# Kernel tuning notes

Measured on AMD Instinct MI355X. Metric: run time of the kernel, lower is better.

The kernel has to match this reference:

```python
import jax, jax.numpy as jnp
import numpy as np

# Nemotron-H Mamba2 mixer decoder layer (prefill path, zero initial states,
# full context lengths). Dims per init_kwargs.
B, S, H = 1, 256, 4096
NH, P, G, N, K = 128, 64, 8, 128, 4   # num_heads, head_dim, n_groups, ssm_state_size, conv_kernel
D_INNER = NH * P                      # 8192
D_STATE = G * N                       # 1024
CONV_DIM = D_INNER + 2 * D_STATE      # 10240
IN_OUT = D_INNER + CONV_DIM + NH      # 18560
EPS = 1e-6


def setup_inputs() -> dict:
    key = jax.random.key(0)
    ks = jax.random.split(key, 8)
    sc = 0.02
    return {
        "hidden_states": jax.random.normal(ks[0], (B, S, H), jnp.float32),
        "conv_state": jnp.zeros((B, CONV_DIM, K - 1), jnp.float32),
        "ssm_state": jnp.zeros((B, NH, P, N), jnp.float32),
        "norm_weight": jnp.ones((H,), jnp.float32),
        "w_in": jax.random.normal(ks[1], (IN_OUT, H), jnp.float32) * sc,
        "conv_w": jax.random.normal(ks[2], (CONV_DIM, K), jnp.float32) * 0.2,
        "conv_b": jnp.zeros((CONV_DIM,), jnp.float32),
        "A_log": jax.random.uniform(ks[3], (NH,), jnp.float32, 0.0, 1.0),
        "D_param": jax.random.normal(ks[4], (NH,), jnp.float32) * 0.1,
        "dt_bias": jax.random.normal(ks[5], (NH,), jnp.float32) * 0.1,
        "ssm_norm_weight": jnp.ones((D_INNER,), jnp.float32),
        "w_out": jax.random.normal(ks[6], (H, D_INNER), jnp.float32) * sc,
    }


def _rmsnorm(x, w, eps=EPS):
    var = jnp.mean(x * x, axis=-1, keepdims=True)
    return x * jax.lax.rsqrt(var + eps) * w


def reference(hidden_states, conv_state, ssm_state, norm_weight, w_in, conv_w,
              conv_b, A_log, D_param, dt_bias, ssm_norm_weight, w_out):
    resid = hidden_states
    h = _rmsnorm(hidden_states, norm_weight)           # pre-mixer RMSNorm
    proj = jnp.einsum('bsh,oh->bso', h, w_in)          # in_proj [B,S,18560]
    gate = proj[..., :D_INNER]
    xconv = proj[..., D_INNER:D_INNER + CONV_DIM]
    dt = proj[..., D_INNER + CONV_DIM:]                # [B,S,NH]

    # depthwise causal conv1d, initial left context = conv_state
    xc = jnp.swapaxes(xconv, 1, 2)                     # [B,CONV_DIM,S]
    xpad = jnp.concatenate([conv_state, xc], axis=-1)  # [B,CONV_DIM,S+K-1]
    conv_state_out = xpad[:, :, -(K - 1):]
    y = conv_b[None, :, None]
    for j in range(K):                                 # K=4 taps, unrolled
        y = y + conv_w[:, j][None, :, None] * xpad[:, :, j:j + S]
    y = jax.nn.silu(jnp.swapaxes(y, 1, 2))             # [B,S,CONV_DIM]

    xs = y[..., :D_INNER].reshape(B, S, NH, P)
    Bs = y[..., D_INNER:D_INNER + D_STATE].reshape(B, S, G, N)
    Cs = y[..., D_INNER + D_STATE:].reshape(B, S, G, N)

    A = -jnp.exp(A_log)                                # [NH]
    dtp = jax.nn.softplus(dt + dt_bias)                # [B,S,NH]
    rep = NH // G
    Bh = jnp.repeat(Bs, rep, axis=2)                   # [B,S,NH,N]
    Ch = jnp.repeat(Cs, rep, axis=2)

    def step(state, inp):
        x_t, b_t, c_t, dt_t = inp                      # [B,NH,P],[B,NH,N],[B,NH,N],[B,NH]
        dA = jnp.exp(dt_t * A)                         # [B,NH]
        state = state * dA[..., None, None] + (dt_t[..., None] * x_t)[..., None] * b_t[:, :, None, :]
        y_t = jnp.einsum('bhpn,bhn->bhp', state, c_t)
        return state, y_t

    inps = (jnp.swapaxes(xs, 0, 1), jnp.swapaxes(Bh, 0, 1),
            jnp.swapaxes(Ch, 0, 1), jnp.swapaxes(dtp, 0, 1))
    ssm_state_out, ys = jax.lax.scan(step, ssm_state, inps)
    ys = jnp.swapaxes(ys, 0, 1) + D_param[None, None, :, None] * xs
    ssm_out = ys.reshape(B, S, D_INNER)

    # gated grouped RMSNorm (group_size = D_INNER // G = 1024)
    gated = ssm_out * jax.nn.silu(gate)
    gsize = D_INNER // G
    gg = gated.reshape(B, S, D_INNER // gsize, gsize)
    var = jnp.mean(gg * gg, axis=-1, keepdims=True)
    normed = (gg * jax.lax.rsqrt(var + EPS)).reshape(B, S, D_INNER) * ssm_norm_weight

    out = jnp.einsum('bsd,hd->bsh', normed, w_out)     # out_proj
    return resid + out, conv_state_out, ssm_state_out
```

## Files before the change

### kernel.cpp

```cpp
#include <hip/hip_runtime.h>
#include <hip/hip_bf16.h>

#define Sq 256
#define Hd 4096
#define NH 128
#define Pd 64
#define Gg 8
#define Nn 128
#define D_INNER 8192
#define D_STATE 1024
#define CONV_DIM 10240
#define IN_OUT 18560
#define DT_COL0 18432
#define EPSI 1e-6f

typedef _Float16 f16x8 __attribute__((ext_vector_type(8)));
typedef _Float16 f16x2 __attribute__((ext_vector_type(2)));
typedef float f32x4 __attribute__((ext_vector_type(4)));

__device__ inline ushort f2h(float f) {
  _Float16 h = (_Float16)f;
  return __builtin_bit_cast(ushort, h);
}
__device__ inline float h2f(ushort u) {
  return (float)__builtin_bit_cast(_Float16, u);
}
__device__ inline ushort f2h_lo(float f, ushort hi) {
  float hf = (float)__builtin_bit_cast(_Float16, hi);
  _Float16 l = (_Float16)(f - hf);
  return __builtin_bit_cast(ushort, l);
}
__device__ inline f16x2 pkrtz(float a, float b) {
  return __builtin_bit_cast(f16x2, __builtin_amdgcn_cvt_pkrtz(a, b));
}

__global__ __launch_bounds__(256) void rmsnorm_k(const float* __restrict__ x,
                                                 const float* __restrict__ w,
                                                 ushort* __restrict__ h_hi,
                                                 ushort* __restrict__ h_lo) {
  int s = blockIdx.x, t = threadIdx.x;
  const float4* row = reinterpret_cast<const float4*>(x + (size_t)s * Hd);
  const float4* wv  = reinterpret_cast<const float4*>(w);
  float4 v[4];
  float ss = 0.f;
#pragma unroll
  for (int i = 0; i < 4; i++) {
    v[i] = row[t + i * 256];
    ss += v[i].x * v[i].x + v[i].y * v[i].y + v[i].z * v[i].z + v[i].w * v[i].w;
  }
#pragma unroll
  for (int off = 32; off > 0; off >>= 1) ss += __shfl_xor(ss, off);
  __shared__ float red[4];
  if ((t & 63) == 0) red[t >> 6] = ss;
  __syncthreads();
  ss = red[0] + red[1] + red[2] + red[3];
  float scale = rsqrtf(ss * (1.f / (float)Hd) + EPSI);
  ushort4* hh = reinterpret_cast<ushort4*>(h_hi + (size_t)s * Hd);
  ushort4* hl = reinterpret_cast<ushort4*>(h_lo + (size_t)s * Hd);
#pragma unroll
  for (int i = 0; i < 4; i++) {
    float4 wi = wv[t + i * 256];
    float f0 = v[i].x * scale * wi.x, f1 = v[i].y * scale * wi.y;
    float f2 = v[i].z * scale * wi.z, f3 = v[i].w * scale * wi.w;
    ushort4 oh, ol;
    oh.x = f2h(f0); ol.x = f2h_lo(f0, oh.x);
    oh.y = f2h(f1); ol.y = f2h_lo(f1, oh.y);
    oh.z = f2h(f2); ol.z = f2h_lo(f2, oh.z);
    oh.w = f2h(f3); ol.w = f2h_lo(f3, oh.w);
    hh[t + i * 256] = oh;
    hl[t + i * 256] = ol;
  }
}

__global__ __launch_bounds__(512) void gemm_8p(const ushort* __restrict__ A,
                                               const float* __restrict__ B,
                                               float* __restrict__ C0,
                                               ushort* __restrict__ Cp,
                                               int ldc, int K, int kLen) {
  __shared__ __align__(16) ushort As[2][256 * 64];
  __shared__ __align__(16) ushort Bs[2][64 * 64];
  int t = threadIdx.x;
  int wave = t >> 6, lane = t & 63;
  int wr = wave >> 1, wc = wave & 1;
  int frow = lane & 15, gq = lane >> 4;
  int bcol = blockIdx.x * 64;
  int z = blockIdx.z;
  int kStart = z * kLen;

  int agl = (lane & 7) ^ (lane >> 3);
  const ushort* ApG = A + (size_t)(wave * 8 + (lane >> 3)) * K + kStart + agl * 8;

  int brow = t >> 3, bgp = t & 7;
  int bgl = bgp ^ (brow & 7);
  const float* BpG = B + (size_t)(bcol + brow) * K + kStart + bgl * 8;
  int bDst = brow * 128 + bgp * 16;

  f32x4 acc[4][2] = {};
  float4 rb[2];
  const int NT = kLen / 64;

#define SB() __builtin_amdgcn_sched_barrier(0)
#define ISSUE_RB(kk) { rb[0] = *(const float4*)(BpG + (kk)); \
                       rb[1] = *(const float4*)(BpG + (kk) + 4); }
#define DMA_A4(buf, kk) { _Pragma("unroll") for (int p = 0; p < 4; ++p) \
    __builtin_amdgcn_global_load_lds( \
        (const __attribute__((address_space(1))) void*)(ApG + (size_t)p * 64 * K + (kk)), \
        (__attribute__((address_space(3))) void*)((char*)&As[0][0] + (buf) * 32768 + p * 8192 + wave * 1024), \
        16, 0, 0); }
#define WRITE_RB(buf) { union { f16x2 h2[4]; uint4 q; } u; \
    u.h2[0] = pkrtz(rb[0].x, rb[0].y); u.h2[1] = pkrtz(rb[0].z, rb[0].w); \
    u.h2[2] = pkrtz(rb[1].x, rb[1].y); u.h2[3] = pkrtz(rb[1].z, rb[1].w); \
    *(uint4*)((char*)&Bs[0][0] + (buf) * 8192 + bDst) = u.q; }
#define PHASE(cur, kh) { \
    f16x8 afp[4], bfp[2]; \
    _Pragma("unroll") for (int m = 0; m < 4; ++m) { \
      int row = wr * 64 + m * 16 + frow; \
      afp[m] = *(const f16x8*)((const char*)&As[0][0] + (cur) * 32768 + row * 128 + \
                               (((((kh) << 2) | gq) ^ (row & 7)) << 4)); } \
    _Pragma("unroll") for (int n = 0; n < 2; ++n) { \
      int row = wc * 32 + n * 16 + frow; \
      bfp[n] = *(const f16x8*)((const char*)&Bs[0][0] + (cur) * 8192 + row * 128 + \
                               (((((kh) << 2) | gq) ^ (row & 7)) << 4)); } \
    asm volatile("s_waitcnt lgkmcnt(0)" ::: "memory"); \
    SB(); \
    __builtin_amdgcn_s_setprio(1); \
    _Pragma("unroll") for (int m = 0; m < 4; ++m) \
      _Pragma("unroll") for (int n = 0; n < 2; ++n) \
        acc[m][n] = __builtin_amdgcn_mfma_f32_16x16x32_f16(afp[m], bfp[n], acc[m][n], 0, 0, 0); \
    __builtin_amdgcn_s_setprio(0); \
    SB(); \
    __builtin_amdgcn_s_barrier(); \
    SB(); }

  ISSUE_RB(0)
  DMA_A4(0, 0)
  WRITE_RB(0)
  __syncthreads();

  for (int i = 0; i < NT; ++i) {
    int cur = i & 1, nxt = cur ^ 1;
    bool nx = (i + 1 < NT);
    if (nx) { ISSUE_RB((i + 1) * 64) DMA_A4(nxt, (i + 1) * 64) }
    SB();
    if (nx) { asm volatile("s_waitcnt vmcnt(6)" ::: "memory"); }
    else    { asm volatile("s_waitcnt vmcnt(0)" ::: "memory"); }
    SB();
    __builtin_amdgcn_s_barrier();
    SB();
    PHASE(cur, 0)
    if (nx) WRITE_RB(nxt)
    PHASE(cur, 1)
  }
#undef SB
#undef ISSUE_RB
#undef DMA_A4
#undef WRITE_RB
#undef PHASE

  if (z == 0) {
#pragma unroll
    for (int m = 0; m < 4; ++m) {
      int row0 = wr * 64 + m * 16 + (lane >> 4) * 4;
#pragma unroll
      for (int n = 0; n < 2; ++n) {
        int col = bcol + wc * 32 + n * 16 + frow;
#pragma unroll
        for (int r = 0; r < 4; ++r)
          C0[(size_t)(row0 + r) * ldc + col] = acc[m][n][r];
      }
    }
  } else {
    ushort* Cz = Cp + (size_t)(z - 1) * Sq * ldc;
#pragma unroll
    for (int m = 0; m < 4; ++m) {
      int row0 = wr * 64 + m * 16 + (lane >> 4) * 4;
#pragma unroll
      for (int n = 0; n < 2; ++n) {
        int col = bcol + wc * 32 + n * 16 + frow;
#pragma unroll
        for (int r = 0; r < 4; ++r)
          Cz[(size_t)(row0 + r) * ldc + col] = f2h(acc[m][n][r]);
      }
    }
  }
}

template<int BN, bool SPLIT>
__global__ __launch_bounds__(256) void gemm_mfma(const ushort* __restrict__ A_hi,
                                                 const ushort* __restrict__ A_lo,
                                                 const float* __restrict__ B,
                                                 float* __restrict__ C,
                                                 int ldc, int K, int kLen,
                                                 int bcol0, int M) {
  constexpr int BK = 64;
  constexpr int LDA = 72;
  constexpr int N_REP = BN / 32;
  constexpr int BQN = (BN == 128) ? 8 : 4;
  __shared__ __align__(16) ushort As[64 * LDA];
  __shared__ __align__(16) ushort Bs[BN * LDA];
  __shared__ __align__(16) ushort AsL[SPLIT ? 64 * LDA : 1];
  __shared__ __align__(16) ushort BsL[SPLIT ? BN * LDA : 1];

  int t = threadIdx.x;
  int wave = t >> 6, lane = t & 63;
  int wr = wave >> 1, wc = wave & 1;
  int frow = lane & 15, fk = (lane >> 4) * 8;
  int rowBase = blockIdx.x * 64;
  int bcol = bcol0 + blockIdx.y * BN;
  int ccol = blockIdx.y * BN;
  int kStart = blockIdx.z * kLen;
  C += (size_t)blockIdx.z * M * ldc;

  int arow = t >> 2, ak = (t & 3) * 16;
  const ushort* Ap  = A_hi + (size_t)(rowBase + arow) * K + ak;
  const ushort* ApL = SPLIT ? (A_lo + (size_t)(rowBase + arow) * K + ak) : nullptr;

  int brow, bq;
  if constexpr (BN == 128) { brow = t >> 1; bq = (t & 1) * 32; }
  else                     { brow = t >> 2; bq = (t & 3) * 16; }
  const float* Bp = B + (size_t)(bcol + brow) * K + bq;

  f32x4 acc[2][N_REP] = {};
  uint4 aPre[2], aPreL[2];
  float4 bPre[BQN];

  auto loadK = [&](int kk) {
    aPre[0] = *reinterpret_cast<const uint4*>(Ap + kk);
    aPre[1] = *reinterpret_cast<const uint4*>(Ap + kk + 8);
    if constexpr (SPLIT) {
      aPreL[0] = *reinterpret_cast<const uint4*>(ApL + kk);
      aPreL[1] = *reinterpret_cast<const uint4*>(ApL + kk + 8);
    }
#pragma unroll
    for (int j = 0; j < BQN; ++j)
      bPre[j] = *reinterpret_cast<const float4*>(Bp + kk + j * 4);
  };

  loadK(kStart);
  for (int ki = 0; ki < kLen; ki += BK) {
    __syncthreads();
    *reinterpret_cast<uint4*>(&As[arow * LDA + ak])     = aPre[0];
    *reinterpret_cast<uint4*>(&As[arow * LDA + ak + 8]) = aPre[1];
    if constexpr (SPLIT) {
      *reinterpret_cast<uint4*>(&AsL[arow * LDA + ak])     = aPreL[0];
      *reinterpret_cast<uint4*>(&AsL[arow * LDA + ak + 8]) = aPreL[1];
    }
    {
      ushort hb[BQN * 4];
      ushort lb[SPLIT ? BQN * 4 : 1];
      const float* bf = reinterpret_cast<const float*>(bPre);
#pragma unroll
      for (int j = 0; j < BQN * 4; ++j) {
        hb[j] = f2h(bf[j]);
        if constexpr (SPLIT) lb[j] = f2h_lo(bf[j], hb[j]);
      }
#pragma unroll
      for (int j = 0; j < BQN / 2; ++j)
        *reinterpret_cast<uint4*>(&Bs[brow * LDA + bq + j * 8]) =
            reinterpret_cast<const uint4*>(hb)[j];
      if constexpr (SPLIT) {
#pragma unroll
        for (int j = 0; j < BQN / 2; ++j)
          *reinterpret_cast<uint4*>(&BsL[brow * LDA + bq + j * 8]) =
              reinterpret_cast<const uint4*>(lb)[j];
      }
    }
    __syncthreads();
    if (ki + BK < kLen) loadK(kStart + ki + BK);
    f16x8 af[2][2], bfv[N_REP][2];
    f16x8 afL[SPLIT ? 2 : 1][2], bfL[SPLIT ? N_REP : 1][2];
#pragma unroll
    for (int m = 0; m < 2; ++m)
#pragma unroll
      for (int kh = 0; kh < 2; ++kh) {
        af[m][kh] = *reinterpret_cast<const f16x8*>(
            &As[(wr * 32 + m * 16 + frow) * LDA + kh * 32 + fk]);
        if constexpr (SPLIT)
          afL[m][kh] = *reinterpret_cast<const f16x8*>(
              &AsL[(wr * 32 + m * 16 + frow) * LDA + kh * 32 + fk]);
      }
#pragma unroll
    for (int n = 0; n < N_REP; ++n)
#pragma unroll
      for (int kh = 0; kh < 2; ++kh) {
        bfv[n][kh] = *reinterpret_cast<const f16x8*>(
            &Bs[(wc * (BN / 2) + n * 16 + frow) * LDA + kh * 32 + fk]);
        if constexpr (SPLIT)
          bfL[n][kh] = *reinterpret_cast<const f16x8*>(
              &BsL[(wc * (BN / 2) + n * 16 + frow) * LDA + kh * 32 + fk]);
      }
#pragma unroll
    for (int kh = 0; kh < 2; ++kh)
#pragma unroll
      for (int m = 0; m < 2; ++m)
#pragma unroll
        for (int n = 0; n < N_REP; ++n) {
          acc[m][n] = __builtin_amdgcn_mfma_f32_16x16x32_f16(af[m][kh], bfv[n][kh], acc[m][n], 0, 0, 0);
          if constexpr (SPLIT) {
            acc[m][n] = __builtin_amdgcn_mfma_f32_16x16x32_f16(af[m][kh], bfL[n][kh], acc[m][n], 0, 0, 0);
            acc[m][n] = __builtin_amdgcn_mfma_f32_16x16x32_f16(afL[m][kh], bfv[n][kh], acc[m][n], 0, 0, 0);
          }
        }
  }

#pragma unroll
  for (int m = 0; m < 2; ++m) {
    int row0 = rowBase + wr * 32 + m * 16 + (lane >> 4) * 4;
#pragma unroll
    for (int n = 0; n < N_REP; ++n) {
      int col = ccol + wc * (BN / 2) + n * 16 + frow;
#pragma unroll
      for (int r = 0; r < 4; ++r)
        C[(size_t)(row0 + r) * ldc + col] = acc[m][n][r];
    }
  }
}

__global__ __launch_bounds__(256) void reduce_in_k(float* __restrict__ proj,
                                                   const ushort* __restrict__ pp) {
  int i = blockIdx.x * 256 + threadIdx.x;
  const size_t PL = (size_t)Sq * IN_OUT;
  float4 o = reinterpret_cast<const float4*>(proj)[i];
#pragma unroll
  for (int zz = 0; zz < 3; ++zz) {
    ushort4 hv = reinterpret_cast<const ushort4*>(pp + zz * PL)[i];
    o.x += h2f(hv.x); o.y += h2f(hv.y); o.z += h2f(hv.z); o.w += h2f(hv.w);
  }
  reinterpret_cast<float4*>(proj)[i] = o;
}

__global__ __launch_bounds__(256) void conv_silu_k(const float* __restrict__ proj,
                                                   const float* __restrict__ cstate,
                                                   const float* __restrict__ cw,
                                                   const float* __restrict__ cb,
                                                   float* __restrict__ y,
                                                   float* __restrict__ out1) {
  int s = blockIdx.y;
  if (s == Sq) {
    int c = blockIdx.x * 256 + threadIdx.x;
#pragma unroll
    for (int tt = 0; tt < 3; ++tt)
      out1[c * 3 + tt] = proj[(size_t)(Sq - 3 + tt) * IN_OUT + D_INNER + c];
    return;
  }
  int c = blockIdx.x * 256 + threadIdx.x;
  float acc = cb[c];
  float4 w4 = *reinterpret_cast<const float4*>(cw + c * 4);
  float wj[4] = {w4.x, w4.y, w4.z, w4.w};
#pragma unroll
  for (int j = 0; j < 4; j++) {
    int si = s + j - 3;
    float v = (si < 0) ? cstate[c * 3 + (si + 3)]
                       : proj[(size_t)si * IN_OUT + D_INNER + c];
    acc += wj[j] * v;
  }
  float sig = 1.f / (1.f + expf(-acc));
  y[(size_t)s * CONV_DIM + c] = acc * sig;
}

#define CS 16
__global__ __launch_bounds__(256) void ssm_scan_k(const float* __restrict__ y_conv,
                                                  const float* __restrict__ dtfix,
                                                  const float* __restrict__ dt_bias,
                                                  const float* __restrict__ sstate_in,
                                                  const float* __restrict__ A_log,
                                                  const float* __restrict__ D_param,
                                                  float* __restrict__ ys_out,
                                                  float* __restrict__ sstate_out) {
  int h = blockIdx.x >> 2;
  int pb = (blockIdx.x & 3) * 16;
  int t = threadIdx.x;
  int ng = t & 15, pl = t >> 4;
  int g = h >> 4;
  float A = -expf(A_log[h]);
  float Dp = D_param[h];
  float bias = dt_bias[h];

  float st[8];
  {
    const float* sp = sstate_in + ((size_t)h * Pd + pb + pl) * Nn + ng * 8;
    float4 v = *reinterpret_cast<const float4*>(sp);
    float4 w = *reinterpret_cast<const float4*>(sp + 4);
    st[0] = v.x; st[1] = v.y; st[2] = v.z; st[3] = v.w;
    st[4] = w.x; st[5] = w.y; st[6] = w.z; st[7] = w.w;
  }

  __shared__ __align__(16) float ybuf[CS][272];
  __shared__ float dts[CS];
  int lr = t >> 4;
  int lc = t & 15;

  for (int ch = 0; ch < Sq / CS; ++ch) {
    int s0 = ch * CS;
    __syncthreads();
    const float* rowp = y_conv + (size_t)(s0 + lr) * CONV_DIM;
#pragma unroll
    for (int j = 0; j < 5; ++j) {
      int c = lc + 16 * j;
      if (c < 68) {
        const float* src;
        int off;
        if (c < 4)       { src = rowp + h * 64 + pb;                      off = c * 4; }
        else if (c < 36) { src = rowp + D_INNER + g * 128;                off = (c - 4) * 4; }
        else             { src = rowp + D_INNER + D_STATE + g * 128;      off = (c - 36) * 4; }
        int dst = (c < 4) ? c * 4 : (c < 36 ? 16 + (c - 4) * 4 : 144 + (c - 36) * 4);
        *reinterpret_cast<float4*>(&ybuf[lr][dst]) = *reinterpret_cast<const float4*>(src + off);
      }
    }
    if (t < CS) {
      float v = bias;
      int idx = (s0 + t) * NH + h;
#pragma unroll
      for (int zz = 0; zz < 32; ++zz) v += dtfix[zz * (Sq * NH) + idx];
      dts[t] = (v > 20.f) ? v : log1pf(expf(v));
    }
    __syncthreads();

#pragma unroll 4
    for (int stp = 0; stp < CS; ++stp) {
      float dt = dts[stp];
      float dA = expf(dt * A);
      float x0 = ybuf[stp][pl];
      float dtx = dt * x0;
      float4 b0 = *reinterpret_cast<const float4*>(&ybuf[stp][16 + ng * 8]);
      float4 b1 = *reinterpret_cast<const float4*>(&ybuf[stp][16 + ng * 8 + 4]);
      float4 c0 = *reinterpret_cast<const float4*>(&ybuf[stp][144 + ng * 8]);
      float4 c1 = *reinterpret_cast<const float4*>(&ybuf[stp][144 + ng * 8 + 4]);
      float y0;
      st[0] = st[0] * dA + dtx * b0.x;  y0  = st[0] * c0.x;
      st[1] = st[1] * dA + dtx * b0.y;  y0 += st[1] * c0.y;
      st[2] = st[2] * dA + dtx * b0.z;  y0 += st[2] * c0.z;
      st[3] = st[3] * dA + dtx * b0.w;  y0 += st[3] * c0.w;
      st[4] = st[4] * dA + dtx * b1.x;  y0 += st[4] * c1.x;
      st[5] = st[5] * dA + dtx * b1.y;  y0 += st[5] * c1.y;
      st[6] = st[6] * dA + dtx * b1.z;  y0 += st[6] * c1.z;
      st[7] = st[7] * dA + dtx * b1.w;  y0 += st[7] * c1.w;
      y0 += __shfl_xor(y0, 1); y0 += __shfl_xor(y0, 2);
      y0 += __shfl_xor(y0, 4); y0 += __shfl_xor(y0, 8);
      if (ng == 0)
        ys_out[(size_t)(s0 + stp) * D_INNER + h * 64 + pb + pl] = y0 + Dp * x0;
    }
  }

  float* so = sstate_out + ((size_t)h * Pd + pb + pl) * Nn + ng * 8;
  *reinterpret_cast<float4*>(so)     = make_float4(st[0], st[1], st[2], st[3]);
  *reinterpret_cast<float4*>(so + 4) = make_float4(st[4], st[5], st[6], st[7]);
}

__global__ __launch_bounds__(256) void gated_norm_k(const float* __restrict__ ys,
                                                    const float* __restrict__ proj,
                                                    const float* __restrict__ w,
                                                    ushort* __restrict__ out_h) {
  int s = blockIdx.x, g = blockIdx.y, t = threadIdx.x;
  float vals[4];
  float ss = 0.f;
#pragma unroll
  for (int i = 0; i < 4; i++) {
    int d = g * 1024 + i * 256 + t;
    float gate = proj[(size_t)s * IN_OUT + d];
    float v = ys[(size_t)s * D_INNER + d] * (gate / (1.f + expf(-gate)));
    vals[i] = v;
    ss += v * v;
  }
#pragma unroll
  for (int off = 32; off > 0; off >>= 1) ss += __shfl_xor(ss, off);
  __shared__ float red[4];
  if ((t & 63) == 0) red[t >> 6] = ss;
  __syncthreads();
  ss = red[0] + red[1] + red[2] + red[3];
  float scale = rsqrtf(ss * (1.f / 1024.f) + EPSI);
#pragma unroll
  for (int i = 0; i < 4; i++) {
    int d = g * 1024 + i * 256 + t;
    out_h[(size_t)s * D_INNER + d] = f2h(vals[i] * scale * w[d]);
  }
}

__global__ __launch_bounds__(256) void reduce_out_k(const float* __restrict__ p0,
                                                    const ushort* __restrict__ pph,
                                                    const float* __restrict__ hidden,
                                                    float* __restrict__ out0) {
  int i = blockIdx.x * 256 + threadIdx.x;
  const size_t PL = (size_t)Sq * Hd;
  float4 o = reinterpret_cast<const float4*>(hidden)[i];
  float4 a = reinterpret_cast<const float4*>(p0)[i];
  o.x += a.x; o.y += a.y; o.z += a.z; o.w += a.w;
#pragma unroll
  for (int zz = 0; zz < 15; ++zz) {
    ushort4 hv = reinterpret_cast<const ushort4*>(pph + zz * PL)[i];
    o.x += h2f(hv.x); o.y += h2f(hv.y); o.z += h2f(hv.z); o.w += h2f(hv.w);
  }
  reinterpret_cast<float4*>(out0)[i] = o;
}

extern "C" void kernel_launch(void* const* d_in, const int* in_sizes, int n_in,
                              void* d_out, int out_size, void* d_ws, size_t ws_size,
                              hipStream_t stream) {
  const float* hidden    = (const float*)d_in[0];
  const float* cstate_in = (const float*)d_in[1];
  const float* sstate_in = (const float*)d_in[2];
  const float* norm_w    = (const float*)d_in[3];
  const float* w_in      = (const float*)d_in[4];
  const float* conv_w    = (const float*)d_in[5];
  const float* conv_b    = (const float*)d_in[6];
  const float* A_log     = (const float*)d_in[7];
  const float* D_param   = (const float*)d_in[8];
  const float* dt_bias   = (const float*)d_in[9];
  const float* ssm_nw    = (const float*)d_in[10];
  const float* w_out     = (const float*)d_in[11];

  float* out0 = (float*)d_out;
  float* out1 = out0 + (size_t)Sq * Hd;
  float* out2 = out1 + (size_t)CONV_DIM * 3;

  ushort* h_hi  = (ushort*)d_ws;
  ushort* h_lo  = h_hi + (size_t)Sq * Hd;
  float*  proj  = (float*)(h_lo + (size_t)Sq * Hd);
  ushort* pp_in = (ushort*)(proj + (size_t)Sq * IN_OUT);
  float*  y_conv = (float*)pp_in;
  float*  dtp   = y_conv + (size_t)Sq * CONV_DIM;
  float*  ys    = dtp + (size_t)Sq * NH;
  ushort* ys_h  = (ushort*)(ys + (size_t)Sq * D_INNER);
  float*  dtfix = (float*)(ys_h + (size_t)Sq * D_INNER);
  float*  op0    = (float*)d_ws;
  ushort* pp_out = (ushort*)(op0 + (size_t)Sq * Hd);

  rmsnorm_k<<<Sq, 256, 0, stream>>>(hidden, norm_w, h_hi, h_lo);
  gemm_8p<<<dim3(IN_OUT / 64, 1, 4), 512, 0, stream>>>(
      h_hi, w_in, proj, pp_in, IN_OUT, Hd, Hd / 4);
  reduce_in_k<<<(Sq * IN_OUT / 4) / 256, 256, 0, stream>>>(proj, pp_in);
  gemm_mfma<64, true><<<dim3(4, 2, 32), 256, 0, stream>>>(
      h_hi, h_lo, w_in, dtfix, NH, Hd, Hd / 32, DT_COL0, Sq);
  conv_silu_k<<<dim3(CONV_DIM / 256, Sq + 1), 256, 0, stream>>>(
      proj, cstate_in, conv_w, conv_b, y_conv, out1);
  ssm_scan_k<<<NH * 4, 256, 0, stream>>>(y_conv, dtfix, dt_bias, sstate_in,
                                         A_log, D_param, ys, out2);
  gated_norm_k<<<dim3(Sq, Gg), 256, 0, stream>>>(ys, proj, ssm_nw, ys_h);
  gemm_8p<<<dim3(Hd / 64, 1, 16), 512, 0, stream>>>(
      ys_h, w_out, op0, pp_out, Hd, D_INNER, D_INNER / 16);
  reduce_out_k<<<(Sq * Hd / 4) / 256, 256, 0, stream>>>(op0, pp_out, hidden, out0);
}
```

Measured before the change: 323.6 us.

## Deepen B-operand prefetch to two stages and halve out_proj split-K

Restructures the gemm_8p main loop so the fp32 B tile loads are issued two K-steps ahead, using alternating register buffers and a loop unrolled by two. A fragments are loaded once per step and reused across both N halves. The in-LDS B write for the next tile is placed between the two MFMA half-phases. Separately, the out_proj GEMM split-K factor drops from 16 to 8, which halves the partial buffers the reduction kernel reads but also halves the grid's block count. The unroll by two assumes NT is even, and the extra register buffers raise register pressure.

```diff
diff --git a/kernel.cpp b/kernel.cpp
--- a/kernel.cpp
+++ b/kernel.cpp
@@ -96,66 +96,94 @@
   int bDst = brow * 128 + bgp * 16;
 
   f32x4 acc[4][2] = {};
-  float4 rb[2];
+  float4 rb0[2], rb1[2];
   const int NT = kLen / 64;
 
 #define SB() __builtin_amdgcn_sched_barrier(0)
-#define ISSUE_RB(kk) { rb[0] = *(const float4*)(BpG + (kk)); \
-                       rb[1] = *(const float4*)(BpG + (kk) + 4); }
+#define ISSUE0(kk) { rb0[0] = *(const float4*)(BpG + (kk)); \
+                     rb0[1] = *(const float4*)(BpG + (kk) + 4); }
+#define ISSUE1(kk) { rb1[0] = *(const float4*)(BpG + (kk)); \
+                     rb1[1] = *(const float4*)(BpG + (kk) + 4); }
 #define DMA_A4(buf, kk) { _Pragma("unroll") for (int p = 0; p < 4; ++p) \
     __builtin_amdgcn_global_load_lds( \
         (const __attribute__((address_space(1))) void*)(ApG + (size_t)p * 64 * K + (kk)), \
         (__attribute__((address_space(3))) void*)((char*)&As[0][0] + (buf) * 32768 + p * 8192 + wave * 1024), \
         16, 0, 0); }
-#define WRITE_RB(buf) { union { f16x2 h2[4]; uint4 q; } u; \
-    u.h2[0] = pkrtz(rb[0].x, rb[0].y); u.h2[1] = pkrtz(rb[0].z, rb[0].w); \
-    u.h2[2] = pkrtz(rb[1].x, rb[1].y); u.h2[3] = pkrtz(rb[1].z, rb[1].w); \
+#define WRITE0(buf) { union { f16x2 h2[4]; uint4 q; } u; \
+    u.h2[0] = pkrtz(rb0[0].x, rb0[0].y); u.h2[1] = pkrtz(rb0[0].z, rb0[0].w); \
+    u.h2[2] = pkrtz(rb0[1].x, rb0[1].y); u.h2[3] = pkrtz(rb0[1].z, rb0[1].w); \
     *(uint4*)((char*)&Bs[0][0] + (buf) * 8192 + bDst) = u.q; }
-#define PHASE(cur, kh) { \
-    f16x8 afp[4], bfp[2]; \
-    _Pragma("unroll") for (int m = 0; m < 4; ++m) { \
-      int row = wr * 64 + m * 16 + frow; \
-      afp[m] = *(const f16x8*)((const char*)&As[0][0] + (cur) * 32768 + row * 128 + \
-                               (((((kh) << 2) | gq) ^ (row & 7)) << 4)); } \
-    _Pragma("unroll") for (int n = 0; n < 2; ++n) { \
-      int row = wc * 32 + n * 16 + frow; \
-      bfp[n] = *(const f16x8*)((const char*)&Bs[0][0] + (cur) * 8192 + row * 128 + \
-                               (((((kh) << 2) | gq) ^ (row & 7)) << 4)); } \
+#define WRITE1(buf) { union { f16x2 h2[4]; uint4 q; } u; \
+    u.h2[0] = pkrtz(rb1[0].x, rb1[0].y); u.h2[1] = pkrtz(rb1[0].z, rb1[0].w); \
+    u.h2[2] = pkrtz(rb1[1].x, rb1[1].y); u.h2[3] = pkrtz(rb1[1].z, rb1[1].w); \
+    *(uint4*)((char*)&Bs[0][0] + (buf) * 8192 + bDst) = u.q; }
+#define STEP(ii, ISS, WRT) { \
+    int cur = (ii) & 1, nxt = cur ^ 1; \
+    bool n1 = (ii) + 1 < NT, n2 = (ii) + 2 < NT; \
+     \
+    if (n2) ISS(((ii) + 2) * 64) \
+    if (n1) DMA_A4(nxt, ((ii) + 1) * 64) \
+    SB(); \
+    if (n2)      { asm volatile("s_waitcnt vmcnt(6)" ::: "memory"); } \
+    else if (n1) { asm volatile("s_waitcnt vmcnt(4)" ::: "memory"); } \
+    else         { asm volatile("s_waitcnt vmcnt(0)" ::: "memory"); } \
+    SB(); \
+    __builtin_amdgcn_s_barrier(); \
+    SB(); \
+    f16x8 af[4][2], bfp[2]; \
+    _Pragma("unroll") for (int m = 0; m < 4; ++m) \
+      _Pragma("unroll") for (int kh = 0; kh < 2; ++kh) { \
+        int row = wr * 64 + m * 16 + frow; \
+        af[m][kh] = *(const f16x8*)((const char*)&As[0][0] + cur * 32768 + row * 128 + \
+                                    ((((kh << 2) | gq) ^ (row & 7)) << 4)); } \
+    { int row = wc * 32 + frow; \
+      _Pragma("unroll") for (int kh = 0; kh < 2; ++kh) \
+        bfp[kh] = *(const f16x8*)((const char*)&Bs[0][0] + cur * 8192 + row * 128 + \
+                                  ((((kh << 2) | gq) ^ (row & 7)) << 4)); } \
     asm volatile("s_waitcnt lgkmcnt(0)" ::: "memory"); \
     SB(); \
     __builtin_amdgcn_s_setprio(1); \
-    _Pragma("unroll") for (int m = 0; m < 4; ++m) \
-      _Pragma("unroll") for (int n = 0; n < 2; ++n) \
-        acc[m][n] = __builtin_amdgcn_mfma_f32_16x16x32_f16(afp[m], bfp[n], acc[m][n], 0, 0, 0); \
+    _Pragma("unroll") for (int kh = 0; kh < 2; ++kh) \
+      _Pragma("unroll") for (int m = 0; m < 4; ++m) \
+        acc[m][0] = __builtin_amdgcn_mfma_f32_16x16x32_f16(af[m][kh], bfp[kh], acc[m][0], 0, 0, 0); \
+    __builtin_amdgcn_s_setprio(0); \
+    SB(); \
+    __builtin_amdgcn_s_barrier(); \
+    SB(); \
+     \
+    if (n1) WRT(nxt) \
+    { int row = wc * 32 + 16 + frow; \
+      _Pragma("unroll") for (int kh = 0; kh < 2; ++kh) \
+        bfp[kh] = *(const f16x8*)((const char*)&Bs[0][0] + cur * 8192 + row * 128 + \
+                                  ((((kh << 2) | gq) ^ (row & 7)) << 4)); } \
+    asm volatile("s_waitcnt lgkmcnt(0)" ::: "memory"); \
+    SB(); \
+    __builtin_amdgcn_s_setprio(1); \
+    _Pragma("unroll") for (int kh = 0; kh < 2; ++kh) \
+      _Pragma("unroll") for (int m = 0; m < 4; ++m) \
+        acc[m][1] = __builtin_amdgcn_mfma_f32_16x16x32_f16(af[m][kh], bfp[kh], acc[m][1], 0, 0, 0); \
     __builtin_amdgcn_s_setprio(0); \
     SB(); \
     __builtin_amdgcn_s_barrier(); \
     SB(); }
 
-  ISSUE_RB(0)
+  ISSUE0(0)
   DMA_A4(0, 0)
-  WRITE_RB(0)
+  WRITE0(0)
+  if (NT > 1) ISSUE1(64)
   __syncthreads();
 
-  for (int i = 0; i < NT; ++i) {
-    int cur = i & 1, nxt = cur ^ 1;
-    bool nx = (i + 1 < NT);
-    if (nx) { ISSUE_RB((i + 1) * 64) DMA_A4(nxt, (i + 1) * 64) }
-    SB();
-    if (nx) { asm volatile("s_waitcnt vmcnt(6)" ::: "memory"); }
-    else    { asm volatile("s_waitcnt vmcnt(0)" ::: "memory"); }
-    SB();
-    __builtin_amdgcn_s_barrier();
-    SB();
-    PHASE(cur, 0)
-    if (nx) WRITE_RB(nxt)
-    PHASE(cur, 1)
+  for (int i = 0; i < NT; i += 2) {
+    STEP(i,     ISSUE0, WRITE1)
+    STEP(i + 1, ISSUE1, WRITE0)
   }
 #undef SB
-#undef ISSUE_RB
+#undef ISSUE0
+#undef ISSUE1
 #undef DMA_A4
-#undef WRITE_RB
-#undef PHASE
+#undef WRITE0
+#undef WRITE1
+#undef STEP
 
   if (z == 0) {
 #pragma unroll
@@ -486,7 +514,7 @@
   float4 a = reinterpret_cast<const float4*>(p0)[i];
   o.x += a.x; o.y += a.y; o.z += a.z; o.w += a.w;
 #pragma unroll
-  for (int zz = 0; zz < 15; ++zz) {
+  for (int zz = 0; zz < 7; ++zz) {
     ushort4 hv = reinterpret_cast<const ushort4*>(pph + zz * PL)[i];
     o.x += h2f(hv.x); o.y += h2f(hv.y); o.z += h2f(hv.z); o.w += h2f(hv.w);
   }
@@ -536,7 +564,7 @@
   ssm_scan_k<<<NH * 4, 256, 0, stream>>>(y_conv, dtfix, dt_bias, sstate_in,
                                          A_log, D_param, ys, out2);
   gated_norm_k<<<dim3(Sq, Gg), 256, 0, stream>>>(ys, proj, ssm_nw, ys_h);
-  gemm_8p<<<dim3(Hd / 64, 1, 16), 512, 0, stream>>>(
-      ys_h, w_out, op0, pp_out, Hd, D_INNER, D_INNER / 16);
+  gemm_8p<<<dim3(Hd / 64, 1, 8), 512, 0, stream>>>(
+      ys_h, w_out, op0, pp_out, Hd, D_INNER, D_INNER / 8);
   reduce_out_k<<<(Sq * Hd / 4) / 256, 256, 0, stream>>>(op0, pp_out, hidden, out0);
 }
```

Result: slower. 334.6 us (+3.4%).
